# Kernel optimization log

Hardware: AMD Instinct MI355X
Metric: run time of the kernel (lower is better)

## Reference

```python
import jax, jax.numpy as jnp
import numpy as np

MAX_OOV = 50

def setup_inputs() -> dict:
    key = jax.random.key(0)
    ks = jax.random.split(key, 20)
    B, T, Tc, E, H, V = 128, 256, 200, 256, 512, 50000
    s = 0.02
    inp = {
        'input': jax.random.randint(ks[0], (B, 1), 0, V),
        'h0': jax.random.normal(ks[1], (1, B, H), jnp.float32),
        'c0': jax.random.normal(ks[2], (1, B, H), jnp.float32),
        'encoder_outputs': jax.random.normal(ks[3], (B, T, H), jnp.float32),
        'context_encoder_outputs': jax.random.normal(ks[4], (B, Tc, H), jnp.float32),
        'context_input': jax.random.randint(ks[5], (B, Tc), 0, V + MAX_OOV),
        'embedding': jax.random.normal(ks[6], (V, E), jnp.float32) * s,
        'W_ih': jax.random.normal(ks[7], (4 * H, E), jnp.float32) * s,
        'W_hh': jax.random.normal(ks[8], (4 * H, H), jnp.float32) * s,
        'b_ih': jnp.zeros((4 * H,), jnp.float32),
        'b_hh': jnp.zeros((4 * H,), jnp.float32),
        'attn_W': jax.random.normal(ks[9], (H, H), jnp.float32) * s,
        'attn_b': jnp.zeros((H,), jnp.float32),
        'cattn_W': jax.random.normal(ks[10], (H, H), jnp.float32) * s,
        'cattn_b': jnp.zeros((H,), jnp.float32),
        'gen_W': jax.random.normal(ks[11], (1, 3 * H + E), jnp.float32) * s,
        'gen_b': jnp.zeros((1,), jnp.float32),
        'sig_b': jax.random.uniform(ks[12], (1,), jnp.float32, -0.1, 0.1),
        'out_W': jax.random.normal(ks[13], (V, H), jnp.float32) * s,
        'out_b': jnp.zeros((V,), jnp.float32),
    }
    return inp

def reference(input, h0, c0, encoder_outputs, context_encoder_outputs, context_input,
              embedding, W_ih, W_hh, b_ih, b_hh, attn_W, attn_b, cattn_W, cattn_b,
              gen_W, gen_b, sig_b, out_W, out_b):
    B = input.shape[0]
    V = out_W.shape[0]
    Vext = V + MAX_OOV
    # embedding lookup (input_len == 1)
    emb = embedding[input[:, 0]]                       # [B, E]
    # single-step LSTM (PyTorch gate order: i, f, g, o)
    gates = emb @ W_ih.T + b_ih + h0[0] @ W_hh.T + b_hh  # [B, 4H]
    i, f, g, o = jnp.split(gates, 4, axis=-1)
    c1 = jax.nn.sigmoid(f) * c0[0] + jax.nn.sigmoid(i) * jnp.tanh(g)
    h1 = jax.nn.sigmoid(o) * jnp.tanh(c1)              # [B, H]
    output = h1
    # attention over encoder_outputs (context_only)
    dec = output @ attn_W.T + attn_b                   # [B, H]
    scores = jax.nn.softmax(jnp.einsum('bth,bh->bt', encoder_outputs, dec), axis=1)
    context = jnp.einsum('bt,bth->bh', scores, encoder_outputs)
    # context attention (score_only)
    cdec = output @ cattn_W.T + cattn_b
    cscores = jax.nn.softmax(jnp.einsum('bth,bh->bt', context_encoder_outputs, cdec), axis=1)  # [B, Tc]
    cctx = jnp.einsum('bt,bth->bh', cscores, context_encoder_outputs)
    # generation probability
    feats = jnp.concatenate([context, cctx, output, emb], axis=1)  # [B, 3H+E]
    p_gen = jax.nn.sigmoid(feats @ gen_W.T + gen_b + sig_b)        # [B, 1]
    ctx_len = (context_input > 0).sum(axis=1, keepdims=True)
    p_gen = jnp.where(ctx_len == 0, jnp.float32(1.0), p_gen)
    # vocab distribution, extended with oov zeros
    p_vocab = jax.nn.softmax(output @ out_W.T + out_b, axis=1)
    p_vocab = jnp.concatenate([p_vocab, jnp.zeros((B, MAX_OOV), p_vocab.dtype)], axis=1)
    # copy distribution: scatter-add attention scores into extended vocab
    p_copy = jnp.zeros((B, Vext), p_vocab.dtype).at[
        jnp.arange(B)[:, None], context_input].add(cscores)
    prob = p_gen * p_vocab + (1.0 - p_gen) * p_copy
    logp = jnp.log(jnp.clip(prob, 1e-10))
    return logp, (h1[None], c1[None])
```

## Files before the change

kernel.cpp:

```cpp
#include <hip/hip_runtime.h>
#include <hip/hip_bf16.h>

#define BB 128
#define T_ENC 256
#define T_CTX 200
#define E_DIM 256
#define H_DIM 512
#define V_DIM 50000
#define N_OOV 50
#define VEXT  50050
#define FOURH 2048
#define K_GATES 768
#define LOGP_SZ (BB * VEXT)
#define OUT_H1_OFF LOGP_SZ
#define OUT_C1_OFF (LOGP_SZ + BB * H_DIM)
#define VCHUNK 2048
#define NCHUNK 25
#define NBIG 782
#define MSP_PITCH 784

typedef __bf16 bf16x8 __attribute__((ext_vector_type(8)));
typedef float  floatx4 __attribute__((ext_vector_type(4)));

__device__ __forceinline__ float wave_sum(float v) {
#pragma unroll
  for (int m = 32; m > 0; m >>= 1) v += __shfl_xor(v, m, 64);
  return v;
}

__device__ __forceinline__ float sigm(float x) { return 1.0f / (1.0f + __expf(-x)); }

__device__ __forceinline__ unsigned f2bf2(float a, float b) {
  unsigned ua = __float_as_uint(a), ub = __float_as_uint(b);
  ua = (ua + 0x7FFFu + ((ua >> 16) & 1u)) >> 16;
  ub = (ub + 0x7FFFu + ((ub >> 16) & 1u)) & 0xFFFF0000u;
  return ua | ub;
}

__global__ __launch_bounds__(256) void prep_all(
    const float* __restrict__ W_ih, const float* __restrict__ W_hh,
    const float* __restrict__ attnW, const float* __restrict__ cattnW,
    const float* __restrict__ attnb, const float* __restrict__ cattnb,
    const int* __restrict__ input, const float* __restrict__ embT,
    const float* __restrict__ h0,
    __bf16* __restrict__ Wcat, __bf16* __restrict__ Wattn, float* __restrict__ attnbc,
    __bf16* __restrict__ Abuf, float* __restrict__ embf) {
  int n = blockIdx.x, tid = threadIdx.x;
  if (n < 2048) {
    unsigned* wr = (unsigned*)(Wcat + (size_t)n * K_GATES);
    for (int idx = tid; idx < 384; idx += 256) {
      int e0 = idx * 2;
      float2 x = (e0 < 256) ? *(const float2*)(W_ih + (size_t)n * E_DIM + e0)
                            : *(const float2*)(W_hh + (size_t)n * H_DIM + e0 - 256);
      wr[idx] = f2bf2(x.x, x.y);
    }
    if (n < 1024) {
      const float* src = (n < 512) ? (attnW + (size_t)n * H_DIM) : (cattnW + (size_t)(n - 512) * H_DIM);
      unsigned* wa = (unsigned*)(Wattn + (size_t)n * H_DIM);
      float2 x = *(const float2*)(src + tid * 2);
      wa[tid] = f2bf2(x.x, x.y);
    }
    if (n < 4) {
      int i = n * 256 + tid;
      attnbc[i] = (i < 512) ? attnb[i] : cattnb[i - 512];
    }
  } else {
    int b = n - 2048;
    int tok = input[b];
    unsigned* ar = (unsigned*)(Abuf + (size_t)b * K_GATES);
    for (int idx = tid; idx < 384; idx += 256) {
      int e0 = idx * 2;
      float2 x;
      if (e0 < 256) {
        x = *(const float2*)(embT + (size_t)tok * E_DIM + e0);
        *(float2*)(embf + b * E_DIM + e0) = x;
      } else {
        x = *(const float2*)(h0 + (size_t)b * H_DIM + e0 - 256);
      }
      ar[idx] = f2bf2(x.x, x.y);
    }
  }
}

template <int BF32, int STATS>
__device__ __forceinline__ void gemm64_body(
    __bf16 (* __restrict__ As)[72], __bf16 (* __restrict__ Bs)[72],
    const __bf16* __restrict__ Abf, const void* __restrict__ Bsrc,
    const float* __restrict__ bias, float* __restrict__ C,
    int n0, int N, int Koff, int Klen, int Kpitch, size_t ldc,
    float2* __restrict__ mspart, int cb) {
  int tid = threadIdx.x, lane = tid & 63, wid = tid >> 6;

  floatx4 acc[2][4];
#pragma unroll
  for (int i = 0; i < 2; i++)
#pragma unroll
    for (int j = 0; j < 4; j++) acc[i][j] = (floatx4){0.f, 0.f, 0.f, 0.f};

  int arow = tid >> 1, ahalf = tid & 1;
  int brow = tid >> 2, bq = tid & 3;
  int gnb = n0 + brow; if (gnb > N - 1) gnb = N - 1;

  const __bf16* abase = Abf + (size_t)arow * Kpitch + Koff + ahalf * 32;
  const float*  bfb = (const float*)Bsrc + (size_t)gnb * Kpitch + Koff + bq * 16;
  const __bf16* bhb = (const __bf16*)Bsrc + (size_t)gnb * Kpitch + Koff + bq * 16;

  uint4 ra[4];
  float4 rbf[4];
  uint4 rbh[2];
  {
    const uint4* s = (const uint4*)abase;
    ra[0] = s[0]; ra[1] = s[1]; ra[2] = s[2]; ra[3] = s[3];
    if (BF32) { const float4* t = (const float4*)bfb; rbf[0] = t[0]; rbf[1] = t[1]; rbf[2] = t[2]; rbf[3] = t[3]; }
    else      { const uint4* t = (const uint4*)bhb;  rbh[0] = t[0]; rbh[1] = t[1]; }
  }

  for (int k0 = 0; k0 < Klen; k0 += 64) {
    __syncthreads();
    { uint4* d = (uint4*)&As[arow][ahalf * 32]; d[0] = ra[0]; d[1] = ra[1]; d[2] = ra[2]; d[3] = ra[3]; }
    if (BF32) {
      uint4 o0, o1;
      o0.x = f2bf2(rbf[0].x, rbf[0].y); o0.y = f2bf2(rbf[0].z, rbf[0].w);
      o0.z = f2bf2(rbf[1].x, rbf[1].y); o0.w = f2bf2(rbf[1].z, rbf[1].w);
      o1.x = f2bf2(rbf[2].x, rbf[2].y); o1.y = f2bf2(rbf[2].z, rbf[2].w);
      o1.z = f2bf2(rbf[3].x, rbf[3].y); o1.w = f2bf2(rbf[3].z, rbf[3].w);
      uint4* d = (uint4*)&Bs[brow][bq * 16]; d[0] = o0; d[1] = o1;
    } else {
      uint4* d = (uint4*)&Bs[brow][bq * 16]; d[0] = rbh[0]; d[1] = rbh[1];
    }
    if (k0 + 64 < Klen) {
      const uint4* s = (const uint4*)(abase + k0 + 64);
      ra[0] = s[0]; ra[1] = s[1]; ra[2] = s[2]; ra[3] = s[3];
      if (BF32) { const float4* t = (const float4*)(bfb + k0 + 64); rbf[0] = t[0]; rbf[1] = t[1]; rbf[2] = t[2]; rbf[3] = t[3]; }
      else      { const uint4* t = (const uint4*)(bhb + k0 + 64);  rbh[0] = t[0]; rbh[1] = t[1]; }
    }
    __syncthreads();
#pragma unroll
    for (int kk = 0; kk < 64; kk += 32) {
      int kbase = kk + (lane >> 4) * 8;
      bf16x8 a0 = *(const bf16x8*)&As[wid * 32 + (lane & 15)][kbase];
      bf16x8 a1 = *(const bf16x8*)&As[wid * 32 + 16 + (lane & 15)][kbase];
      bf16x8 bfr[4];
#pragma unroll
      for (int j = 0; j < 4; j++) bfr[j] = *(const bf16x8*)&Bs[j * 16 + (lane & 15)][kbase];
#pragma unroll
      for (int j = 0; j < 4; j++) {
        acc[0][j] = __builtin_amdgcn_mfma_f32_16x16x32_bf16(a0, bfr[j], acc[0][j], 0, 0, 0);
        acc[1][j] = __builtin_amdgcn_mfma_f32_16x16x32_bf16(a1, bfr[j], acc[1][j], 0, 0, 0);
      }
    }
  }
  int cn = lane & 15, cq = lane >> 4;
#pragma unroll
  for (int i = 0; i < 2; i++)
#pragma unroll
    for (int j = 0; j < 4; j++)
#pragma unroll
      for (int r = 0; r < 4; r++) {
        int row = wid * 32 + i * 16 + cq * 4 + r;
        int col = n0 + j * 16 + cn;
        if (col < N) {
          float v = acc[i][j][r];
          if (bias) v += bias[col];
          C[(size_t)row * ldc + col] = v;
        }
      }
  if (STATS) {
#pragma unroll
    for (int i = 0; i < 2; i++)
#pragma unroll
      for (int r = 0; r < 4; r++) {
        int row = wid * 32 + i * 16 + cq * 4 + r;
        float v[4]; float mx = -1e30f;
#pragma unroll
        for (int j = 0; j < 4; j++) {
          int col = n0 + j * 16 + cn;
          float x = acc[i][j][r] + bias[col < N ? col : N - 1];
          v[j] = (col < N) ? x : -1e30f;
          mx = fmaxf(mx, v[j]);
        }
#pragma unroll
        for (int mk = 1; mk <= 8; mk <<= 1) mx = fmaxf(mx, __shfl_xor(mx, mk, 64));
        float s = 0.f;
#pragma unroll
        for (int j = 0; j < 4; j++) s += (v[j] > -1e29f) ? __expf(v[j] - mx) : 0.f;
#pragma unroll
        for (int mk = 1; mk <= 8; mk <<= 1) s += __shfl_xor(s, mk, 64);
        if (cn == 0) mspart[(size_t)row * MSP_PITCH + cb] = make_float2(mx, s);
      }
  }
}

__global__ __launch_bounds__(256) void gates_gemm(
    const __bf16* __restrict__ Abuf, const __bf16* __restrict__ Wcat,
    float* __restrict__ g0, float* __restrict__ g1) {
  __shared__ __bf16 As[128][72];
  __shared__ __bf16 Bs[64][72];
  int bx = blockIdx.x;
  int kh = bx >> 5, nb = bx & 31;
  gemm64_body<0, 0>(As, Bs, Abuf, Wcat, nullptr, kh ? g1 : g0, nb * 64, FOURH,
                    kh * 384, 384, K_GATES, FOURH, nullptr, 0);
}

__global__ __launch_bounds__(256) void mega_gemm(
    const __bf16* __restrict__ h1b, const float* __restrict__ outW,
    const float* __restrict__ outb, float* __restrict__ logits, size_t lpitch,
    const __bf16* __restrict__ Wattn, const float* __restrict__ attnbc,
    float* __restrict__ decbuf, float2* __restrict__ mspart) {
  __shared__ __bf16 As[128][72];
  __shared__ __bf16 Bs[64][72];
  int bx = blockIdx.x;
  if (bx < NBIG)
    gemm64_body<1, 1>(As, Bs, h1b, outW, outb, logits, bx * 64, V_DIM,
                      0, H_DIM, H_DIM, lpitch, mspart, bx);
  else
    gemm64_body<0, 0>(As, Bs, h1b, Wattn, attnbc, decbuf, (bx - NBIG) * 64, 1024,
                      0, H_DIM, H_DIM, 1024, nullptr, 0);
}

__global__ __launch_bounds__(256) void lstm_kernel(
    const float* __restrict__ gA, const float* __restrict__ gB,
    const float* __restrict__ b_ih, const float* __restrict__ b_hh,
    const float* __restrict__ c0,
    float* __restrict__ h1_out, float* __restrict__ c1_out, __bf16* __restrict__ h1b) {
  int idx = blockIdx.x * 256 + threadIdx.x;
  int b = idx >> 9, j = idx & 511;
  const float* ga = gA + b * FOURH;
  const float* gb = gB + b * FOURH;
  float iv = ga[j]        + gb[j]        + b_ih[j]        + b_hh[j];
  float fv = ga[512 + j]  + gb[512 + j]  + b_ih[512 + j]  + b_hh[512 + j];
  float gv = ga[1024 + j] + gb[1024 + j] + b_ih[1024 + j] + b_hh[1024 + j];
  float ov = ga[1536 + j] + gb[1536 + j] + b_ih[1536 + j] + b_hh[1536 + j];
  float c1 = sigm(fv) * c0[idx] + sigm(iv) * tanhf(gv);
  float h1 = sigm(ov) * tanhf(c1);
  h1_out[idx] = h1;
  c1_out[idx] = c1;
  h1b[idx] = (__bf16)h1;
}

__global__ __launch_bounds__(256) void flash_kernel(
    const float* __restrict__ enc, const float* __restrict__ cenc,
    const float* __restrict__ decbuf, float* __restrict__ opart,
    float2* __restrict__ mlb, float* __restrict__ rawsc) {
  __shared__ float so[4][512];
  __shared__ float sml[4][2];
  int g = blockIdx.x;
  int b = g & 127;
  int cc = g >> 7;
  int which = cc >> 2, chunk = cc & 3;
  int tchunk = which ? 50 : 64;
  int t0 = chunk * tchunk;
  const float* src = which ? (cenc + (size_t)b * T_CTX * H_DIM) : (enc + (size_t)b * T_ENC * H_DIM);
  const float* decp = decbuf + b * 1024 + which * 512;
  int tid = threadIdx.x, lane = tid & 63, wid = tid >> 6;
  float4 d0 = *(const float4*)(decp + lane * 8);
  float4 d1 = *(const float4*)(decp + lane * 8 + 4);
  float m = -1e30f, l = 0.f;
  float4 o0 = {0.f, 0.f, 0.f, 0.f}, o1 = {0.f, 0.f, 0.f, 0.f};
  for (int t = t0 + wid; t < t0 + tchunk; t += 4) {
    const float* row = src + (size_t)t * H_DIM + lane * 8;
    float4 r0 = *(const float4*)row;
    float4 r1 = *(const float4*)(row + 4);
    float p = r0.x * d0.x + r0.y * d0.y + r0.z * d0.z + r0.w * d0.w +
              r1.x * d1.x + r1.y * d1.y + r1.z * d1.z + r1.w * d1.w;
    p = wave_sum(p);
    if (which && lane == 0) rawsc[b * T_CTX + t] = p;
    float mn = fmaxf(m, p);
    float sc = __expf(m - mn);
    float e  = __expf(p - mn);
    l = l * sc + e;
    o0.x = o0.x * sc + e * r0.x; o0.y = o0.y * sc + e * r0.y;
    o0.z = o0.z * sc + e * r0.z; o0.w = o0.w * sc + e * r0.w;
    o1.x = o1.x * sc + e * r1.x; o1.y = o1.y * sc + e * r1.y;
    o1.z = o1.z * sc + e * r1.z; o1.w = o1.w * sc + e * r1.w;
    m = mn;
  }
  *(float4*)&so[wid][lane * 8]     = o0;
  *(float4*)&so[wid][lane * 8 + 4] = o1;
  if (lane == 0) { sml[wid][0] = m; sml[wid][1] = l; }
  __syncthreads();
  float M = fmaxf(fmaxf(sml[0][0], sml[1][0]), fmaxf(sml[2][0], sml[3][0]));
  float w0 = __expf(sml[0][0] - M), w1 = __expf(sml[1][0] - M);
  float w2 = __expf(sml[2][0] - M), w3 = __expf(sml[3][0] - M);
  float L = w0 * sml[0][1] + w1 * sml[1][1] + w2 * sml[2][1] + w3 * sml[3][1];
  int h = tid, h2 = tid + 256;
  float O0 = w0 * so[0][h]  + w1 * so[1][h]  + w2 * so[2][h]  + w3 * so[3][h];
  float O1 = w0 * so[0][h2] + w1 * so[1][h2] + w2 * so[2][h2] + w3 * so[3][h2];
  opart[(size_t)g * 512 + h]  = O0;
  opart[(size_t)g * 512 + h2] = O1;
  if (tid == 0) mlb[g] = make_float2(M, L);
}

__global__ __launch_bounds__(256) void final_kernel(
    const float* __restrict__ logits, size_t lpitch,
    float* __restrict__ out, const int* __restrict__ ctx_inp,
    const float* __restrict__ rawsc, const float2* __restrict__ mlb,
    const float2* __restrict__ mspart, const float* __restrict__ opart,
    const float* __restrict__ h1f, const float* __restrict__ embf,
    const float* __restrict__ genW, const float* __restrict__ genb,
    const float* __restrict__ sigb) {
  __shared__ float pc[VCHUNK];
  __shared__ float sm[256], ss[256];
  __shared__ float red8[8];
  int bx = blockIdx.x;
  int b = bx & 127, c = bx >> 7;
  int tid = threadIdx.x, lane = tid & 63, wid = tid >> 6;
  int cidx = (tid < T_CTX) ? ctx_inp[b * T_CTX + tid] : 0;

  float2 e0 = mlb[b], e1 = mlb[128 + b], e2 = mlb[256 + b], e3 = mlb[384 + b];
  float2 f0 = mlb[512 + b], f1 = mlb[640 + b], f2 = mlb[768 + b], f3 = mlb[896 + b];
  float M0 = fmaxf(fmaxf(e0.x, e1.x), fmaxf(e2.x, e3.x));
  float a0 = __expf(e0.x - M0), a1 = __expf(e1.x - M0), a2 = __expf(e2.x - M0), a3 = __expf(e3.x - M0);
  float L0 = a0 * e0.y + a1 * e1.y + a2 * e2.y + a3 * e3.y;
  float M1 = fmaxf(fmaxf(f0.x, f1.x), fmaxf(f2.x, f3.x));
  float c0_ = __expf(f0.x - M1), c1_ = __expf(f1.x - M1), c2_ = __expf(f2.x - M1), c3_ = __expf(f3.x - M1);
  float L1 = c0_ * f0.y + c1_ * f1.y + c2_ * f2.y + c3_ * f3.y;

  float acc = 0.f;
  for (int j = tid; j < 1792; j += 256) {
    float x;
    if (j < 1024) {
      int which = j >> 9, h = j & 511;
      const float* op = opart + ((size_t)(which * 512 + b) * 512) + h;
      if (which == 0)
        x = (a0 * op[0] + a1 * op[128 * 512] + a2 * op[256 * 512] + a3 * op[384 * 512]) / L0;
      else
        x = (c0_ * op[0] + c1_ * op[128 * 512] + c2_ * op[256 * 512] + c3_ * op[384 * 512]) / L1;
    } else if (j < 1536) x = h1f[b * 512 + j - 1024];
    else x = embf[b * 256 + j - 1536];
    acc += x * genW[j];
  }
  float cnt = (tid < T_CTX && cidx > 0) ? 1.f : 0.f;
  acc = wave_sum(acc); cnt = wave_sum(cnt);
  if (lane == 0) { red8[wid] = acc; red8[4 + wid] = cnt; }

  float m = -1e30f, s = 0.f;
  for (int cb = tid; cb < NBIG; cb += 256) {
    float2 p = mspart[(size_t)b * MSP_PITCH + cb];
    float mo = fmaxf(m, p.x);
    s = s * __expf(m - mo) + p.y * __expf(p.x - mo);
    m = mo;
  }
  sm[tid] = m; ss[tid] = s;
#pragma unroll
  for (int k = 0; k < 8; k++) pc[tid * 8 + k] = 0.f;
  __syncthreads();
  for (int st = 128; st; st >>= 1) {
    if (tid < st) {
      float m2 = sm[tid + st], s2 = ss[tid + st];
      float mo = fmaxf(sm[tid], m2);
      ss[tid] = ss[tid] * __expf(sm[tid] - mo) + s2 * __expf(m2 - mo);
      sm[tid] = mo;
    }
    __syncthreads();
  }
  float rm = sm[0], rs = ss[0];
  float pg;
  {
    float a = red8[0] + red8[1] + red8[2] + red8[3];
    float cn = red8[4] + red8[5] + red8[6] + red8[7];
    pg = sigm(a + genb[0] + sigb[0]);
    if (cn == 0.f) pg = 1.0f;
  }
  int v0c = c * VCHUNK;
  if (tid < T_CTX) {
    int rel = cidx - v0c;
    if (rel >= 0 && rel < VCHUNK) {
      float val = __expf(rawsc[b * T_CTX + tid] - M1) / L1;
      atomicAdd(&pc[rel], val);
    }
  }
  __syncthreads();
  float inv = 1.0f / rs, pc1 = 1.0f - pg;
  const float* rowsrc = logits + (size_t)b * lpitch;
  float* rowdst = out + (size_t)b * VEXT;
  int li0 = tid * 8;
#pragma unroll
  for (int k = 0; k < 4; k++) {
    int li = li0 + 2 * k;
    int v = v0c + li;
    float2 x = *(const float2*)(rowsrc + v);
    float pv0 = (v < V_DIM)     ? __expf(x.x - rm) * inv : 0.f;
    float pv1 = (v + 1 < V_DIM) ? __expf(x.y - rm) * inv : 0.f;
    float r0 = __logf(fmaxf(pg * pv0 + pc1 * pc[li],     1e-10f));
    float r1 = __logf(fmaxf(pg * pv1 + pc1 * pc[li + 1], 1e-10f));
    if (v + 1 < VEXT)      *(float2*)(rowdst + v) = make_float2(r0, r1);
    else if (v < VEXT)     rowdst[v] = r0;
  }
}

extern "C" void kernel_launch(void* const* d_in, const int* in_sizes, int n_in,
                              void* d_out, int out_size, void* d_ws, size_t ws_size,
                              hipStream_t stream) {
  const int*   input   = (const int*)d_in[0];
  const float* h0      = (const float*)d_in[1];
  const float* c0      = (const float*)d_in[2];
  const float* enc     = (const float*)d_in[3];
  const float* cenc    = (const float*)d_in[4];
  const int*   ctx_inp = (const int*)d_in[5];
  const float* embT    = (const float*)d_in[6];
  const float* W_ih    = (const float*)d_in[7];
  const float* W_hh    = (const float*)d_in[8];
  const float* b_ih    = (const float*)d_in[9];
  const float* b_hh    = (const float*)d_in[10];
  const float* attnW   = (const float*)d_in[11];
  const float* attnb   = (const float*)d_in[12];
  const float* cattnW  = (const float*)d_in[13];
  const float* cattnb  = (const float*)d_in[14];
  const float* genW    = (const float*)d_in[15];
  const float* genb    = (const float*)d_in[16];
  const float* sigb    = (const float*)d_in[17];
  const float* outW    = (const float*)d_in[18];
  const float* outb    = (const float*)d_in[19];

  char* ws = (char*)d_ws;
  __bf16* Wcat   = (__bf16*)(ws + 0);
  __bf16* Wattn  = (__bf16*)(ws + 3145728);
  float*  attnbc = (float*)(ws + 4194304);
  __bf16* Abuf   = (__bf16*)(ws + 4198400);
  float*  embf   = (float*)(ws + 4395008);
  float*  gates  = (float*)(ws + 4526080);
  float*  gates2 = (float*)(ws + 5574656);
  __bf16* h1b    = (__bf16*)(ws + 6623232);
  float*  decbuf = (float*)(ws + 6754304);
  float*  opart  = (float*)(ws + 7278592);
  float2* mlb    = (float2*)(ws + 9375744);
  float*  rawsc  = (float*)(ws + 9383936);
  float2* mspart = (float2*)(ws + 9486336);
  const size_t logits_off = 10289152;
  const size_t LPITCH_AL = 50176;

  float* outF = (float*)d_out;
  bool padded = ws_size >= logits_off + (size_t)BB * LPITCH_AL * 4;
  float* logits = padded ? (float*)(ws + logits_off) : outF;
  size_t lpitch = padded ? LPITCH_AL : (size_t)VEXT;

  float* h1_out = outF + OUT_H1_OFF;
  float* c1_out = outF + OUT_C1_OFF;

  prep_all<<<2176, 256, 0, stream>>>(W_ih, W_hh, attnW, cattnW, attnb, cattnb,
                                     input, embT, h0, Wcat, Wattn, attnbc, Abuf, embf);
  gates_gemm<<<64, 256, 0, stream>>>(Abuf, Wcat, gates, gates2);
  lstm_kernel<<<256, 256, 0, stream>>>(gates, gates2, b_ih, b_hh, c0, h1_out, c1_out, h1b);
  mega_gemm<<<NBIG + 16, 256, 0, stream>>>(h1b, outW, outb, logits, lpitch,
                                           Wattn, attnbc, decbuf, mspart);
  flash_kernel<<<1024, 256, 0, stream>>>(enc, cenc, decbuf, opart, mlb, rawsc);
  final_kernel<<<NCHUNK * 128, 256, 0, stream>>>(logits, lpitch, outF, ctx_inp, rawsc, mlb,
                                                 mspart, opart, h1_out, embf, genW, genb, sigb);
}
```

Before: 391.4 us.

## Rewrite mega_gemm to feed MFMA directly from registers with double-buffered loads

Replaces the shared-memory tiled GEMM body in mega_gemm with a register-direct scheme. Each wave loads h1 (bf16) and out_W (fp32, converted to bf16 in registers) straight into MFMA operands, double-buffering the global loads across K steps. Shared memory is used only for a C tile that feeds a coalesced epilogue computing per-block softmax max/sum partials and writing logits. This removes LDS staging and barriers in the K loop, which matters for a skinny M=128 GEMM bound by streaming out_W. In exchange, each block re-reads h1 from global or cache, and register pressure goes up.

```diff
diff --git a/kernel.cpp b/kernel.cpp
--- a/kernel.cpp
+++ b/kernel.cpp
@@ -21,6 +21,7 @@
 
 typedef __bf16 bf16x8 __attribute__((ext_vector_type(8)));
 typedef float  floatx4 __attribute__((ext_vector_type(4)));
+typedef float  floatx2 __attribute__((ext_vector_type(2)));
 
 __device__ __forceinline__ float wave_sum(float v) {
 #pragma unroll
@@ -35,6 +36,17 @@
   ua = (ua + 0x7FFFu + ((ua >> 16) & 1u)) >> 16;
   ub = (ub + 0x7FFFu + ((ub >> 16) & 1u)) & 0xFFFF0000u;
   return ua | ub;
+}
+
+__device__ __forceinline__ bf16x8 u4bf(uint4 u) {
+  union { uint4 a; bf16x8 b; } x; x.a = u; return x.b;
+}
+
+__device__ __forceinline__ bf16x8 cvt8(float4 lo, float4 hi) {
+  bf16x8 r;
+  r[0] = (__bf16)lo.x; r[1] = (__bf16)lo.y; r[2] = (__bf16)lo.z; r[3] = (__bf16)lo.w;
+  r[4] = (__bf16)hi.x; r[5] = (__bf16)hi.y; r[6] = (__bf16)hi.z; r[7] = (__bf16)hi.w;
+  return r;
 }
 
 __global__ __launch_bounds__(256) void prep_all(
@@ -207,15 +219,117 @@
     const float* __restrict__ outb, float* __restrict__ logits, size_t lpitch,
     const __bf16* __restrict__ Wattn, const float* __restrict__ attnbc,
     float* __restrict__ decbuf, float2* __restrict__ mspart) {
-  __shared__ __bf16 As[128][72];
-  __shared__ __bf16 Bs[64][72];
+  __shared__ float ctile[128][68];
   int bx = blockIdx.x;
-  if (bx < NBIG)
-    gemm64_body<1, 1>(As, Bs, h1b, outW, outb, logits, bx * 64, V_DIM,
-                      0, H_DIM, H_DIM, lpitch, mspart, bx);
-  else
-    gemm64_body<0, 0>(As, Bs, h1b, Wattn, attnbc, decbuf, (bx - NBIG) * 64, 1024,
-                      0, H_DIM, H_DIM, 1024, nullptr, 0);
+  int tid = threadIdx.x, lane = tid & 63, wid = tid >> 6;
+  int cn = lane & 15, kq = lane >> 4;
+  const int big = bx < NBIG;
+  int n0 = big ? bx * 64 : (bx - NBIG) * 64;
+  int mycol = n0 + wid * 16 + cn;
+
+  const __bf16* a0 = h1b + (size_t)cn * H_DIM + kq * 8;
+
+  floatx4 acc[8];
+#pragma unroll
+  for (int i = 0; i < 8; ++i) acc[i] = (floatx4){0.f, 0.f, 0.f, 0.f};
+
+  if (big) {
+    int gn = mycol < V_DIM ? mycol : V_DIM - 1;
+    const float* bp = outW + (size_t)gn * H_DIM + kq * 8;
+    uint4  ra[2][8];
+    float4 rb[2][2];
+#pragma unroll
+    for (int i = 0; i < 8; ++i) ra[0][i] = *(const uint4*)(a0 + i * 16 * H_DIM);
+    rb[0][0] = *(const float4*)bp;
+    rb[0][1] = *(const float4*)(bp + 4);
+#pragma unroll
+    for (int s = 0; s < 16; ++s) {
+      const int cur = s & 1, nxt = cur ^ 1;
+      if (s < 15) {
+        int ko = (s + 1) * 32;
+#pragma unroll
+        for (int i = 0; i < 8; ++i) ra[nxt][i] = *(const uint4*)(a0 + i * 16 * H_DIM + ko);
+        rb[nxt][0] = *(const float4*)(bp + ko);
+        rb[nxt][1] = *(const float4*)(bp + ko + 4);
+      }
+      bf16x8 bv = cvt8(rb[cur][0], rb[cur][1]);
+#pragma unroll
+      for (int i = 0; i < 8; ++i)
+        acc[i] = __builtin_amdgcn_mfma_f32_16x16x32_bf16(u4bf(ra[cur][i]), bv, acc[i], 0, 0, 0);
+    }
+    float bcol = outb[gn];
+#pragma unroll
+    for (int i = 0; i < 8; ++i)
+#pragma unroll
+      for (int r = 0; r < 4; ++r)
+        ctile[i * 16 + kq * 4 + r][wid * 16 + cn] = acc[i][r] + bcol;
+  } else {
+    const __bf16* bp = Wattn + (size_t)mycol * H_DIM + kq * 8;
+    uint4 ra[2][8];
+    uint4 rbh[2];
+#pragma unroll
+    for (int i = 0; i < 8; ++i) ra[0][i] = *(const uint4*)(a0 + i * 16 * H_DIM);
+    rbh[0] = *(const uint4*)bp;
+#pragma unroll
+    for (int s = 0; s < 16; ++s) {
+      const int cur = s & 1, nxt = cur ^ 1;
+      if (s < 15) {
+        int ko = (s + 1) * 32;
+#pragma unroll
+        for (int i = 0; i < 8; ++i) ra[nxt][i] = *(const uint4*)(a0 + i * 16 * H_DIM + ko);
+        rbh[nxt] = *(const uint4*)(bp + ko);
+      }
+      bf16x8 bv = u4bf(rbh[cur]);
+#pragma unroll
+      for (int i = 0; i < 8; ++i)
+        acc[i] = __builtin_amdgcn_mfma_f32_16x16x32_bf16(u4bf(ra[cur][i]), bv, acc[i], 0, 0, 0);
+    }
+    float bcol = attnbc[mycol];
+#pragma unroll
+    for (int i = 0; i < 8; ++i)
+#pragma unroll
+      for (int r = 0; r < 4; ++r)
+        ctile[i * 16 + kq * 4 + r][wid * 16 + cn] = acc[i][r] + bcol;
+  }
+  __syncthreads();
+
+  int rr = tid >> 4, c16 = tid & 15;
+  if (big) {
+#pragma unroll
+    for (int p = 0; p < 8; ++p) {
+      int row = p * 16 + rr;
+      int c4 = c16 * 4;
+      int col = n0 + c4;
+      floatx4 v = *(const floatx4*)&ctile[row][c4];
+      float v0 = (col + 0 < V_DIM) ? v[0] : -1e30f;
+      float v1 = (col + 1 < V_DIM) ? v[1] : -1e30f;
+      float v2 = (col + 2 < V_DIM) ? v[2] : -1e30f;
+      float v3 = (col + 3 < V_DIM) ? v[3] : -1e30f;
+      float mx = fmaxf(fmaxf(v0, v1), fmaxf(v2, v3));
+#pragma unroll
+      for (int mk = 1; mk <= 8; mk <<= 1) mx = fmaxf(mx, __shfl_xor(mx, mk, 64));
+      float sum = __expf(v0 - mx) + __expf(v1 - mx) + __expf(v2 - mx) + __expf(v3 - mx);
+#pragma unroll
+      for (int mk = 1; mk <= 8; mk <<= 1) sum += __shfl_xor(sum, mk, 64);
+      if (c16 == 0) mspart[(size_t)row * MSP_PITCH + bx] = make_float2(mx, sum);
+      if (col + 4 <= V_DIM) {
+        float* dst = logits + (size_t)row * lpitch + col;
+        if ((lpitch & 3) == 0) {
+          *(floatx4*)dst = v;
+        } else {
+          *(floatx2*)dst = (floatx2){v[0], v[1]};
+          *(floatx2*)(dst + 2) = (floatx2){v[2], v[3]};
+        }
+      }
+    }
+  } else {
+#pragma unroll
+    for (int p = 0; p < 8; ++p) {
+      int row = p * 16 + rr;
+      floatx4 v = *(const floatx4*)&ctile[row][c16 * 4];
+      *(floatx4*)(decbuf + (size_t)row * 1024 + n0 + c16 * 4) = v;
+    }
+  }
 }
 
 __global__ __launch_bounds__(256) void lstm_kernel(
```

New measurement: 403.3 us. 3.0% more time.

## Specialize vocab GEMM with register prefetch and LDS-staged coalesced epilogue

Applied to the files above, without the earlier changes.

Replaces the generic gemm64_body path for the vocab projection with a specialized kernel body. It prefetches the next K-slice of h1 and out_W into registers while the current slice is multiplied, and converts out_W from fp32 to bf16 on the fly. It stages the accumulator tile through shared memory so the bias add, per-row max/sum partials and logits stores are done with row-contiguous vectorized writes. This targets load latency and uncoalesced output stores, at the cost of more register pressure and a larger shared-memory footprint.

```diff
diff --git a/kernel.cpp b/kernel.cpp
--- a/kernel.cpp
+++ b/kernel.cpp
@@ -21,6 +21,7 @@
 
 typedef __bf16 bf16x8 __attribute__((ext_vector_type(8)));
 typedef float  floatx4 __attribute__((ext_vector_type(4)));
+typedef float  floatx2 __attribute__((ext_vector_type(2)));
 
 __device__ __forceinline__ float wave_sum(float v) {
 #pragma unroll
@@ -207,15 +208,129 @@
     const float* __restrict__ outb, float* __restrict__ logits, size_t lpitch,
     const __bf16* __restrict__ Wattn, const float* __restrict__ attnbc,
     float* __restrict__ decbuf, float2* __restrict__ mspart) {
-  __shared__ __bf16 As[128][72];
-  __shared__ __bf16 Bs[64][72];
+  __shared__ __align__(16) char smem[32768];
+  __bf16 (*As)[72] = (__bf16(*)[72])smem;
+  __bf16 (*Bs)[72] = (__bf16(*)[72])(smem + 18432);
+  float  (*ctile)[64] = (float(*)[64])smem;
+
   int bx = blockIdx.x;
-  if (bx < NBIG)
-    gemm64_body<1, 1>(As, Bs, h1b, outW, outb, logits, bx * 64, V_DIM,
-                      0, H_DIM, H_DIM, lpitch, mspart, bx);
-  else
+  if (bx >= NBIG) {
     gemm64_body<0, 0>(As, Bs, h1b, Wattn, attnbc, decbuf, (bx - NBIG) * 64, 1024,
                       0, H_DIM, H_DIM, 1024, nullptr, 0);
+    return;
+  }
+
+  int tid = threadIdx.x, lane = tid & 63, wid = tid >> 6;
+  int n0 = bx * 64;
+
+  floatx4 acc[2][4];
+#pragma unroll
+  for (int i = 0; i < 2; i++)
+#pragma unroll
+    for (int j = 0; j < 4; j++) acc[i][j] = (floatx4){0.f, 0.f, 0.f, 0.f};
+
+  int arow = tid >> 1, ahalf = tid & 1;
+  int brow = tid >> 2, bq = tid & 3;
+  int gnb = n0 + brow; if (gnb > V_DIM - 1) gnb = V_DIM - 1;
+
+  const __bf16* abase = h1b + (size_t)arow * H_DIM + ahalf * 32;
+  const float*  bfb   = outW + (size_t)gnb * H_DIM + bq * 16;
+
+  uint4 ra[4];
+  float4 rbf[4];
+  {
+    const uint4* s = (const uint4*)abase;
+    ra[0] = s[0]; ra[1] = s[1]; ra[2] = s[2]; ra[3] = s[3];
+    const float4* t = (const float4*)bfb;
+    rbf[0] = t[0]; rbf[1] = t[1]; rbf[2] = t[2]; rbf[3] = t[3];
+  }
+
+  for (int k0 = 0; k0 < H_DIM; k0 += 64) {
+    __syncthreads();
+    { uint4* d = (uint4*)&As[arow][ahalf * 32]; d[0] = ra[0]; d[1] = ra[1]; d[2] = ra[2]; d[3] = ra[3]; }
+    {
+      uint4 o0, o1;
+      o0.x = f2bf2(rbf[0].x, rbf[0].y); o0.y = f2bf2(rbf[0].z, rbf[0].w);
+      o0.z = f2bf2(rbf[1].x, rbf[1].y); o0.w = f2bf2(rbf[1].z, rbf[1].w);
+      o1.x = f2bf2(rbf[2].x, rbf[2].y); o1.y = f2bf2(rbf[2].z, rbf[2].w);
+      o1.z = f2bf2(rbf[3].x, rbf[3].y); o1.w = f2bf2(rbf[3].z, rbf[3].w);
+      uint4* d = (uint4*)&Bs[brow][bq * 16]; d[0] = o0; d[1] = o1;
+    }
+    if (k0 + 64 < H_DIM) {
+      const uint4* s = (const uint4*)(abase + k0 + 64);
+      ra[0] = s[0]; ra[1] = s[1]; ra[2] = s[2]; ra[3] = s[3];
+      const float4* t = (const float4*)(bfb + k0 + 64);
+      rbf[0] = t[0]; rbf[1] = t[1]; rbf[2] = t[2]; rbf[3] = t[3];
+    }
+    __syncthreads();
+#pragma unroll
+    for (int kk = 0; kk < 64; kk += 32) {
+      int kbase = kk + (lane >> 4) * 8;
+      bf16x8 a0 = *(const bf16x8*)&As[wid * 32 + (lane & 15)][kbase];
+      bf16x8 a1 = *(const bf16x8*)&As[wid * 32 + 16 + (lane & 15)][kbase];
+      bf16x8 bfr[4];
+#pragma unroll
+      for (int j = 0; j < 4; j++) bfr[j] = *(const bf16x8*)&Bs[j * 16 + (lane & 15)][kbase];
+#pragma unroll
+      for (int j = 0; j < 4; j++) {
+        acc[0][j] = __builtin_amdgcn_mfma_f32_16x16x32_bf16(a0, bfr[j], acc[0][j], 0, 0, 0);
+        acc[1][j] = __builtin_amdgcn_mfma_f32_16x16x32_bf16(a1, bfr[j], acc[1][j], 0, 0, 0);
+      }
+    }
+  }
+
+  __syncthreads();
+  {
+    int cn = lane & 15, cq = lane >> 4;
+#pragma unroll
+    for (int i = 0; i < 2; i++)
+#pragma unroll
+      for (int j = 0; j < 4; j++)
+#pragma unroll
+        for (int r = 0; r < 4; r++)
+          ctile[wid * 32 + i * 16 + cq * 4 + r][j * 16 + cn] = acc[i][j][r];
+  }
+  __syncthreads();
+
+  int rr = tid >> 4, c16 = tid & 15;
+  int c4 = c16 * 4;
+  int col = n0 + c4;
+  float b0, b1, b2, b3;
+  if (n0 + 64 <= V_DIM) {
+    float4 bb = *(const float4*)(outb + col);
+    b0 = bb.x; b1 = bb.y; b2 = bb.z; b3 = bb.w;
+  } else {
+    b0 = (col + 0 < V_DIM) ? outb[col + 0] : 0.f;
+    b1 = (col + 1 < V_DIM) ? outb[col + 1] : 0.f;
+    b2 = (col + 2 < V_DIM) ? outb[col + 2] : 0.f;
+    b3 = (col + 3 < V_DIM) ? outb[col + 3] : 0.f;
+  }
+#pragma unroll
+  for (int p = 0; p < 8; ++p) {
+    int row = p * 16 + rr;
+    floatx4 v = *(const floatx4*)&ctile[row][c4];
+    v[0] += b0; v[1] += b1; v[2] += b2; v[3] += b3;
+    float v0 = (col + 0 < V_DIM) ? v[0] : -1e30f;
+    float v1 = (col + 1 < V_DIM) ? v[1] : -1e30f;
+    float v2 = (col + 2 < V_DIM) ? v[2] : -1e30f;
+    float v3 = (col + 3 < V_DIM) ? v[3] : -1e30f;
+    float mx = fmaxf(fmaxf(v0, v1), fmaxf(v2, v3));
+#pragma unroll
+    for (int mk = 1; mk <= 8; mk <<= 1) mx = fmaxf(mx, __shfl_xor(mx, mk, 64));
+    float sum = __expf(v0 - mx) + __expf(v1 - mx) + __expf(v2 - mx) + __expf(v3 - mx);
+#pragma unroll
+    for (int mk = 1; mk <= 8; mk <<= 1) sum += __shfl_xor(sum, mk, 64);
+    if (c16 == 0) mspart[(size_t)row * MSP_PITCH + bx] = make_float2(mx, sum);
+    if (col + 4 <= V_DIM) {
+      float* dst = logits + (size_t)row * lpitch + col;
+      if ((lpitch & 3) == 0) {
+        *(floatx4*)dst = v;
+      } else {
+        *(floatx2*)dst = (floatx2){v[0], v[1]};
+        *(floatx2*)(dst + 2) = (floatx2){v[2], v[3]};
+      }
+    }
+  }
 }
 
 __global__ __launch_bounds__(256) void lstm_kernel(
```

New measurement: 389.3 us. About the same (-0.6%).
